# Kernel tuning notes

Hardware: AMD Instinct MI355X
Metric: run time of the kernel (lower is better)

Reference implementation:

```python
import jax, jax.numpy as jnp
import numpy as np

B, S, DIM = 2, 2048, 4096
N_HEADS, N_KV_HEADS = 32, 8
HEAD_DIM = DIM // N_HEADS  # 128
N_REP = N_HEADS // N_KV_HEADS  # 4
NEG_INF = -1e9


def setup_inputs() -> dict:
    key = jax.random.key(0)
    ks = jax.random.split(key, 6)
    x = jax.random.normal(ks[0], (B, S, DIM), dtype=jnp.float32)
    # torch Linear weights are [out_features, in_features]
    sc = 0.02
    wq = jax.random.normal(ks[1], (N_HEADS * HEAD_DIM, DIM), dtype=jnp.float32) * sc
    wk = jax.random.normal(ks[2], (N_KV_HEADS * HEAD_DIM, DIM), dtype=jnp.float32) * sc
    wv = jax.random.normal(ks[3], (N_KV_HEADS * HEAD_DIM, DIM), dtype=jnp.float32) * sc
    wo = jax.random.normal(ks[4], (DIM, N_HEADS * HEAD_DIM), dtype=jnp.float32) * sc
    # RoPE frequencies, matching llama precompute_freqs_cis (theta=10000)
    inv = 1.0 / (10000.0 ** (np.arange(0, HEAD_DIM, 2, dtype=np.float32) / HEAD_DIM))
    t = np.arange(S, dtype=np.float32)
    freqs = np.outer(t, inv)  # [S, HEAD_DIM//2]
    freqs_cos = jnp.asarray(np.cos(freqs), dtype=jnp.float32)
    freqs_sin = jnp.asarray(np.sin(freqs), dtype=jnp.float32)
    # causal mask: 0 on/below diagonal, large negative above
    mask = jnp.triu(jnp.full((S, S), NEG_INF, dtype=jnp.float32), k=1)
    return {"x": x, "wq": wq, "wk": wk, "wv": wv, "wo": wo,
            "freqs_cos": freqs_cos, "freqs_sin": freqs_sin,
            "mask": mask, "start_pos": 0}


def _apply_rope(t, cos, sin):
    # t: [b, s, h, hd]; complex mult on interleaved (even, odd) pairs
    tr, ti = t[..., 0::2], t[..., 1::2]
    cos = cos[None, :, None, :]
    sin = sin[None, :, None, :]
    out_r = tr * cos - ti * sin
    out_i = tr * sin + ti * cos
    return jnp.stack([out_r, out_i], axis=-1).reshape(t.shape)


def reference(x, wq, wk, wv, wo, freqs_cos, freqs_sin, mask, start_pos):
    bsz, seqlen, _ = x.shape
    xq = (x @ wq.T).reshape(bsz, seqlen, N_HEADS, HEAD_DIM)
    xk = (x @ wk.T).reshape(bsz, seqlen, N_KV_HEADS, HEAD_DIM)
    xv = (x @ wv.T).reshape(bsz, seqlen, N_KV_HEADS, HEAD_DIM)
    xq = _apply_rope(xq, freqs_cos, freqs_sin)
    xk = _apply_rope(xk, freqs_cos, freqs_sin)
    # prefill: start_pos == 0, so cache slice == current keys/values
    # GQA repeat_kv via broadcast (torch repeat_interleave over head dim)
    keys = jnp.broadcast_to(xk[:, :, :, None, :],
                            (bsz, seqlen, N_KV_HEADS, N_REP, HEAD_DIM)
                            ).reshape(bsz, seqlen, N_HEADS, HEAD_DIM)
    values = jnp.broadcast_to(xv[:, :, :, None, :],
                              (bsz, seqlen, N_KV_HEADS, N_REP, HEAD_DIM)
                              ).reshape(bsz, seqlen, N_HEADS, HEAD_DIM)
    scale = 1.0 / jnp.sqrt(jnp.float32(HEAD_DIM))
    # [b, h, q, k]
    scores = jnp.einsum('bqhd,bkhd->bhqk', xq, keys) * scale
    scores = scores + mask[None, None, :, :]
    probs = jax.nn.softmax(scores.astype(jnp.float32), axis=-1).astype(xq.dtype)
    out = jnp.einsum('bhqk,bkhd->bqhd', probs, values)
    out = out.reshape(bsz, seqlen, N_HEADS * HEAD_DIM)
    return out @ wo.T
```

## Files before the change

kernel.cpp:

```cpp
#include <hip/hip_runtime.h>

typedef unsigned short u16;
typedef unsigned int u32;
typedef __bf16 bf16_t;
typedef bf16_t bf16x8 __attribute__((ext_vector_type(8)));
typedef float f32x4 __attribute__((ext_vector_type(4)));

#define B_ 2
#define S_ 2048
#define DIM_ 4096
#define NH_ 32
#define NKV_ 8
#define HD_ 128

__device__ __forceinline__ u16 f2b(float f) {
  union { float f; unsigned u; } x; x.f = f;
  unsigned r = x.u + 0x7fffu + ((x.u >> 16) & 1u);
  return (u16)(r >> 16);
}
__device__ __forceinline__ float b2f(u16 u) {
  union { unsigned u; float f; } x; x.u = ((unsigned)u) << 16;
  return x.f;
}
__device__ __forceinline__ u32 cvtpk(float lo, float hi) {
  u32 r;
  asm volatile("v_cvt_pk_bf16_f32 %0, %1, %2" : "=v"(r) : "v"(lo), "v"(hi));
  return r;
}
__device__ __forceinline__ float redmax4(float x) {
  x = fmaxf(x, __shfl_xor(x, 16));
  x = fmaxf(x, __shfl_xor(x, 32));
  return x;
}
__device__ __forceinline__ float redsum4(float x) {
  x += __shfl_xor(x, 16);
  x += __shfl_xor(x, 32);
  return x;
}

#define GLDS(gsrc, ldst) \
  __builtin_amdgcn_global_load_lds((const __attribute__((address_space(1))) void*)(gsrc), \
                                   (__attribute__((address_space(3))) void*)(ldst), 16, 0, 0)
#define BAR()    __builtin_amdgcn_s_barrier()
#define SCHED0() __builtin_amdgcn_sched_barrier(0)

__global__ void cvt_kernel(const float* __restrict__ in, u16* __restrict__ out, int n4) {
  int i = blockIdx.x * blockDim.x + threadIdx.x;
  int stride = gridDim.x * blockDim.x;
  for (; i < n4; i += stride) {
    float4 v = ((const float4*)in)[i];
    ushort4 o;
    o.x = f2b(v.x); o.y = f2b(v.y); o.z = f2b(v.z); o.w = f2b(v.w);
    ((ushort4*)out)[i] = o;
  }
}

__global__ void rope_kernel(u16* __restrict__ t, const float* __restrict__ fc,
                            const float* __restrict__ fs, int nheads) {
  int idx = blockIdx.x * blockDim.x + threadIdx.x;
  int ppr = nheads * 64;
  int row = idx / ppr;
  int pr = idx - row * ppr;
  int h = pr >> 6, j = pr & 63;
  int s = row & (S_ - 1);
  float c = fc[s * 64 + j], sn = fs[s * 64 + j];
  u16* p = t + (size_t)row * (size_t)(nheads * HD_) + h * HD_ + j * 2;
  float tr = b2f(p[0]), ti = b2f(p[1]);
  p[0] = f2b(tr * c - ti * sn);
  p[1] = f2b(tr * sn + ti * c);
}

__global__ __launch_bounds__(512) void attn_kernel(const u16* __restrict__ Q,
                                                   const u16* __restrict__ Kt,
                                                   const u16* __restrict__ VT,
                                                   u16* __restrict__ O,
                                                   const float* __restrict__ fc,
                                                   const float* __restrict__ fs) {
  __shared__ u16 Ks[2][32 * 128];
  __shared__ u16 Vs[2][32 * 128];

  const int bid = blockIdx.x;
  const int qb = 15 - (bid >> 6);
  const int h = bid & 31;
  const int b = (bid >> 5) & 1;
  const int g = h >> 2;
  const int tid = threadIdx.x;
  const int lane = tid & 63;
  const int wv = tid >> 6;
  const int qrow0 = qb * 128 + wv * 16;
  const float scl2 = 0.12751744f;

  const int qloc = lane & 15;
  const int grp = lane >> 4;

  bf16x8 qf[4];
  {
    const int qr = qrow0 + qloc;
    const u16* qptr = Q + (size_t)(b * S_ + qr) * (NH_ * HD_) + h * HD_ + grp * 8;
#pragma unroll
    for (int c = 0; c < 4; c++) {
      union { bf16x8 v; u16 u[8]; } raw;
      raw.v = *(const bf16x8*)(qptr + c * 32);
      const int p0 = c * 16 + grp * 4;
      const float4 cv = *(const float4*)&fc[(size_t)qr * 64 + p0];
      const float4 sv = *(const float4*)&fs[(size_t)qr * 64 + p0];
      union { bf16x8 v; u32 w[4]; } out;
      const float cc[4] = {cv.x, cv.y, cv.z, cv.w};
      const float ss[4] = {sv.x, sv.y, sv.z, sv.w};
#pragma unroll
      for (int j = 0; j < 4; j++) {
        float tr = b2f(raw.u[2 * j]), ti = b2f(raw.u[2 * j + 1]);
        out.w[j] = cvtpk(tr * cc[j] - ti * ss[j], tr * ss[j] + ti * cc[j]);
      }
      qf[c] = out.v;
    }
  }

  float m = -1e30f, l = 0.f;
  f32x4 o[8];
#pragma unroll
  for (int c = 0; c < 8; c++)
#pragma unroll
    for (int r = 0; r < 4; r++) o[c][r] = 0.f;

  const int nkv = 4 * qb + 4;

  int ka[2][4];
#pragma unroll
  for (int n = 0; n < 2; n++)
#pragma unroll
    for (int c = 0; c < 4; c++) {
      int krow = n * 16 + qloc;
      ka[n][c] = krow * 256 + ((c * 64 + grp * 16) ^ ((krow & 7) << 4));
    }
  int va[8];
#pragma unroll
  for (int c = 0; c < 8; c++) {
    int d = c * 16 + qloc;
    va[c] = d * 64 + ((grp * 16) ^ (((d >> 1) & 3) << 4));
  }

  const int kkey = wv * 4 + grp;
  const int cbsK = (qloc * 16) ^ ((kkey & 7) << 4);
  const int vd = wv * 16 + (lane >> 2);
  const int kbsV = ((lane & 3) * 16) ^ (((vd >> 1) & 3) << 4);

  const u16* kp = Kt + (size_t)(b * S_ + kkey) * 1024 + g * HD_ + (cbsK >> 1);
  const u16* vp = VT + (size_t)(g * HD_ + vd) * 4096 + (size_t)b * S_ + (kbsV >> 1);

  GLDS(kp, &Ks[0][wv * 512]);
  GLDS(vp, &Vs[0][wv * 512]);
  kp += 32 * 1024;
  vp += 32;

#define ATTN_ITER(T, CB, NB)                                                   \
  {                                                                            \
    const bool pf = ((T) + 1 < nkv);                                           \
    if (pf) {                                                                  \
      GLDS(kp, &Ks[NB][wv * 512]);                                             \
      GLDS(vp, &Vs[NB][wv * 512]);                                             \
      asm volatile("s_waitcnt vmcnt(2)" ::: "memory");                         \
    } else {                                                                   \
      asm volatile("s_waitcnt vmcnt(0)" ::: "memory");                         \
    }                                                                          \
    BAR();                                                                     \
    SCHED0();                                                                  \
    if ((T) * 32 <= qrow0 + 15) {                                              \
      f32x4 s[2];                                                              \
      __builtin_amdgcn_s_setprio(1);                                           \
      _Pragma("unroll")                                                        \
      for (int n = 0; n < 2; n++) {                                            \
        f32x4 sc;                                                              \
        _Pragma("unroll")                                                      \
        for (int r = 0; r < 4; r++) sc[r] = 0.f;                               \
        _Pragma("unroll")                                                      \
        for (int c = 0; c < 4; c++) {                                          \
          bf16x8 kf = *(const bf16x8*)((const char*)Ks[CB] + ka[n][c]);        \
          sc = __builtin_amdgcn_mfma_f32_16x16x32_bf16(kf, qf[c], sc, 0, 0, 0);\
        }                                                                      \
        s[n] = sc;                                                             \
      }                                                                        \
      __builtin_amdgcn_s_setprio(0);                                           \
      const int q = qrow0 + qloc;                                              \
      if ((T) * 32 + 31 > qrow0) {                                             \
        _Pragma("unroll")                                                      \
        for (int n = 0; n < 2; n++)                                            \
          _Pragma("unroll")                                                    \
          for (int r = 0; r < 4; r++) {                                        \
            int k = (T) * 32 + n * 16 + grp * 4 + r;                           \
            if (k > q) s[n][r] = -1e9f;                                        \
          }                                                                    \
      }                                                                        \
      float pmax = fmaxf(fmaxf(fmaxf(s[0][0], s[0][1]), fmaxf(s[0][2], s[0][3])), \
                         fmaxf(fmaxf(s[1][0], s[1][1]), fmaxf(s[1][2], s[1][3]))); \
      pmax = redmax4(pmax);                                                    \
      if (__any(pmax > m + 64.f)) {                                            \
        float mn = fmaxf(m, pmax);                                             \
        float alpha = exp2f((m - mn) * scl2);                                  \
        m = mn;                                                                \
        l *= alpha;                                                            \
        float ar[4];                                                           \
        _Pragma("unroll")                                                      \
        for (int r = 0; r < 4; r++) ar[r] = __shfl(alpha, grp * 4 + r);        \
        _Pragma("unroll")                                                      \
        for (int c = 0; c < 8; c++)                                            \
          _Pragma("unroll")                                                    \
          for (int r = 0; r < 4; r++) o[c][r] *= ar[r];                        \
      }                                                                        \
      const float msc = m * scl2;                                              \
      float p[2][4];                                                           \
      _Pragma("unroll")                                                        \
      for (int n = 0; n < 2; n++)                                              \
        _Pragma("unroll")                                                      \
        for (int r = 0; r < 4; r++)                                            \
          p[n][r] = exp2f(fmaf(s[n][r], scl2, -msc));                          \
      float rs = ((p[0][0] + p[0][1]) + (p[0][2] + p[0][3])) +                 \
                 ((p[1][0] + p[1][1]) + (p[1][2] + p[1][3]));                  \
      l += redsum4(rs);                                                        \
      u32 a0 = cvtpk(p[0][0], p[0][1]);                                        \
      u32 a1 = cvtpk(p[0][2], p[0][3]);                                        \
      u32 b0 = cvtpk(p[1][0], p[1][1]);                                        \
      u32 b1 = cvtpk(p[1][2], p[1][3]);                                        \
      asm volatile("v_permlane32_swap_b32 %0, %1" : "+v"(a0), "+v"(b0));       \
      asm volatile("v_permlane32_swap_b32 %0, %1" : "+v"(a1), "+v"(b1));       \
      asm volatile("v_permlane16_swap_b32 %0, %1" : "+v"(a0), "+v"(b0));       \
      asm volatile("v_permlane16_swap_b32 %0, %1" : "+v"(a1), "+v"(b1));       \
      union { bf16x8 v; u32 w[4]; } pau;                                       \
      pau.w[0] = a0; pau.w[1] = a1; pau.w[2] = b0; pau.w[3] = b1;              \
      bf16x8 pa = pau.v;                                                       \
      __builtin_amdgcn_s_setprio(1);                                           \
      _Pragma("unroll")                                                        \
      for (int c = 0; c < 8; c++) {                                            \
        bf16x8 vf = *(const bf16x8*)((const char*)Vs[CB] + va[c]);             \
        o[c] = __builtin_amdgcn_mfma_f32_16x16x32_bf16(pa, vf, o[c], 0, 0, 0); \
      }                                                                        \
      __builtin_amdgcn_s_setprio(0);                                           \
    }                                                                          \
    asm volatile("s_waitcnt lgkmcnt(0)" ::: "memory");                         \
    SCHED0();                                                                  \
    BAR();                                                                     \
    kp += 32 * 1024;                                                           \
    vp += 32;                                                                  \
  }

  for (int t = 0; t < nkv; t += 2) {
    ATTN_ITER(t, 0, 1);
    ATTN_ITER(t + 1, 1, 0);
  }
#undef ATTN_ITER

  float lr[4];
#pragma unroll
  for (int r = 0; r < 4; r++) lr[r] = 1.0f / __shfl(l, grp * 4 + r);
#pragma unroll
  for (int c = 0; c < 8; c++)
#pragma unroll
    for (int r = 0; r < 4; r++) {
      int qo = qrow0 + grp * 4 + r;
      float val = o[c][r] * lr[r];
      O[(size_t)(b * S_ + qo) * (NH_ * HD_) + h * HD_ + c * 16 + qloc] = f2b(val);
    }
}

template<int MODE, bool SM>
__global__ __launch_bounds__(512, 2) void gemm256(const u16* __restrict__ A,
                                                  const u16* __restrict__ B,
                                                  void* __restrict__ Cout,
                                                  void* __restrict__ Cout2,
                                                  int M, int N, int K) {
  constexpr int BM = SM ? 128 : 256;
  constexpr int AH = SM ? 4096 : 8192;
  constexpr int II = SM ? 1 : 2;
  constexpr int NACC = SM ? 4 : 8;
  __shared__ u16 As[2][2][AH];
  __shared__ u16 Bs[2][2][8192];
  const int nbn = N >> 8;
  const int nwg = gridDim.x;
  int wg = blockIdx.x;
  wg = (wg & 7) * (nwg >> 3) + (wg >> 3);
  const int bm = wg / nbn;
  const int bn = wg - bm * nbn;
  const int tid = threadIdx.x;
  const int lane = tid & 63;
  const int wv = tid >> 6;
  const int wm = wv >> 2, wn = wv & 3;
  const int qloc = lane & 15, grp = lane >> 4;
  const int NT = K >> 6;

  f32x4 acc[NACC][4];
#pragma unroll
  for (int i = 0; i < NACC; i++)
#pragma unroll
    for (int j = 0; j < 4; j++)
#pragma unroll
      for (int r = 0; r < 4; r++) acc[i][j][r] = 0.0f;

  const int srowl = lane >> 3;
  const int scsw = 8 * ((lane & 7) ^ srowl);
  const size_t rowA = SM ? ((size_t)(bm * 128 + wv * 8 + srowl) * K + scsw)
                         : ((size_t)(bm * 256 + wv * 16 + srowl) * K + scsw);
  const size_t rowB = (size_t)(bn * 256 + wv * 16 + srowl) * K + scsw;

#define STAGE_A(buf, h, tt) { \
    if (SM) { \
      GLDS(A + rowA + (size_t)((h) * 64) * K + (size_t)(tt) * 64, &As[buf][h][wv * 512]); \
    } else { \
      GLDS(A + rowA + (size_t)((h) * 128) * K + (size_t)(tt) * 64, &As[buf][h][wv * 1024]); \
      GLDS(A + rowA + (size_t)((h) * 128 + 8) * K + (size_t)(tt) * 64, &As[buf][h][wv * 1024 + 512]); } }
#define STAGE_B(buf, h, tt) { \
    GLDS(B + rowB + (size_t)((h) * 128) * K + (size_t)(tt) * 64, &Bs[buf][h][wv * 1024]); \
    GLDS(B + rowB + (size_t)((h) * 128 + 8) * K + (size_t)(tt) * 64, &Bs[buf][h][wv * 1024 + 512]); }

  STAGE_A(0, 0, 0); STAGE_A(0, 1, 0);
  STAGE_B(0, 0, 0); STAGE_B(0, 1, 0);
  STAGE_B(1, 0, 1); STAGE_B(1, 1, 1);
  asm volatile("s_waitcnt vmcnt(4)" ::: "memory");
  BAR();

  for (int t = 0; t < NT; t += 2) {
#pragma unroll
    for (int half = 0; half < 2; half++) {
      bf16x8 bfr[4][2];
#pragma unroll
      for (int qd = 0; qd < 4; qd++) {
        if (qd == 0) {
#pragma unroll
          for (int j = 0; j < 4; j++)
#pragma unroll
            for (int ks = 0; ks < 2; ks++) {
              int rb = (wn & 1) * 64 + j * 16 + qloc;
              bfr[j][ks] = *(const bf16x8*)((const char*)&Bs[half][wn >> 1][0]
                           + rb * 128 + ((ks * 64 + grp * 16) ^ ((rb & 7) << 4)));
            }
        }
        bf16x8 af[II][2];
#pragma unroll
        for (int ii = 0; ii < II; ii++)
#pragma unroll
          for (int ks = 0; ks < 2; ks++) {
            int rh = SM ? (qd * 16 + qloc) : (qd * 32 + ii * 16 + qloc);
            af[ii][ks] = *(const bf16x8*)((const char*)&As[half][wm][0]
                         + rh * 128 + ((ks * 64 + grp * 16) ^ ((rh & 7) << 4)));
          }
        BAR();
        asm volatile("s_waitcnt lgkmcnt(0)" ::: "memory");
        SCHED0();
        __builtin_amdgcn_s_setprio(1);
#pragma unroll
        for (int ii = 0; ii < II; ii++)
#pragma unroll
          for (int ks = 0; ks < 2; ks++)
#pragma unroll
            for (int j = 0; j < 4; j++)
              acc[qd * II + ii][j] = __builtin_amdgcn_mfma_f32_16x16x32_bf16(
                  af[ii][ks], bfr[j][ks], acc[qd * II + ii][j], 0, 0, 0);
        __builtin_amdgcn_s_setprio(0);
        SCHED0();
        const int ph = half * 4 + qd;
        if (ph == 0)      { STAGE_A(1, 0, t + 1); STAGE_A(1, 1, t + 1); }
        else if (ph == 1) { if (t + 2 < NT) { STAGE_B(0, 0, t + 2); STAGE_B(0, 1, t + 2); } }
        else if (ph == 4) { if (t + 2 < NT) { STAGE_A(0, 0, t + 2); STAGE_A(0, 1, t + 2); } }
        else if (ph == 5) { if (t + 3 < NT) { STAGE_B(1, 0, t + 3); STAGE_B(1, 1, t + 3); } }
        if (qd == 3) {
          if ((half == 0 ? t + 2 : t + 3) < NT)
            asm volatile("s_waitcnt vmcnt(4)" ::: "memory");
          else
            asm volatile("s_waitcnt vmcnt(0)" ::: "memory");
          BAR();
        }
      }
    }
  }
#undef STAGE_A
#undef STAGE_B

  const int r0g = bm * BM + wm * (BM / 2) + grp * 4;
  const int c0g = bn * 256 + wn * 64 + qloc;
#pragma unroll
  for (int i = 0; i < NACC; i++)
#pragma unroll
    for (int j = 0; j < 4; j++)
#pragma unroll
      for (int r = 0; r < 4; r++) {
        int row = r0g + i * 16 + r;
        int col = c0g + j * 16;
        float v = acc[i][j][r];
        if (MODE == 1)      ((float*)Cout)[(size_t)row * N + col] = v;
        else if (MODE == 0) ((u16*)Cout)[(size_t)row * N + col]  = f2b(v);
        else {
          if (col < 1024) ((u16*)Cout)[(size_t)row * 1024 + col] = f2b(v);
          else            ((u16*)Cout2)[(size_t)(col - 1024) * M + row] = f2b(v);
        }
      }
}

extern "C" void kernel_launch(void* const* d_in, const int* in_sizes, int n_in,
                              void* d_out, int out_size, void* d_ws, size_t ws_size,
                              hipStream_t stream) {
  const float* x  = (const float*)d_in[0];
  const float* wq = (const float*)d_in[1];
  const float* wk = (const float*)d_in[2];
  const float* wv = (const float*)d_in[3];
  const float* wo = (const float*)d_in[4];
  const float* fc = (const float*)d_in[5];
  const float* fs = (const float*)d_in[6];

  char* ws = (char*)d_ws;
  u16* Xb  = (u16*)(ws);
  u16* Wqb = (u16*)(ws + 33554432);
  u16* Wkv = (u16*)(ws + 67108864);
  u16* Qw  = (u16*)(ws + 83886080);
  u16* Kw  = (u16*)(ws + 117440512);
  u16* Vw  = (u16*)(ws + 125829120);
  u16* Ow  = Xb;
  u16* Wob = Wqb;

  auto cvt = [&](const float* in, u16* out, int n) {
    int n4 = n >> 2;
    int blocks = (n4 + 255) / 256; if (blocks > 2048) blocks = 2048;
    cvt_kernel<<<dim3(blocks), dim3(256), 0, stream>>>(in, out, n4);
  };
  cvt(x,  Xb,  B_ * S_ * DIM_);
  cvt(wq, Wqb, DIM_ * DIM_);
  cvt(wk, Wkv, NKV_ * HD_ * DIM_);
  cvt(wv, Wkv + (size_t)1024 * 4096, NKV_ * HD_ * DIM_);

  gemm256<0, false><<<dim3(16 * 16), 512, 0, stream>>>(Xb, Wqb, Qw, nullptr, 4096, 4096, 4096);
  gemm256<3, true><<<dim3(32 * 8), 512, 0, stream>>>(Xb, Wkv, Kw, Vw, 4096, 2048, 4096);

  cvt(wo, Wob, DIM_ * DIM_);

  rope_kernel<<<dim3((B_ * S_ * NKV_ * 64) / 256), 256, 0, stream>>>(Kw, fc, fs, NKV_);

  attn_kernel<<<dim3(B_ * NH_ * (S_ / 128)), 512, 0, stream>>>(Qw, Kw, Vw, Ow, fc, fs);

  gemm256<1, false><<<dim3(16 * 16), 512, 0, stream>>>(Ow, Wob, d_out, nullptr, 4096, 4096, 4096);
}
```

Before: 505.5 us.

## Double KV tile size in attention kernel from 32 to 64 keys

The flash-attention loop now processes 64 keys per iteration instead of 32, so it stages twice as much K and V into shared memory per step and runs half as many iterations. Each barrier pair, softmax rescale check and reduction now covers twice the work, which cuts per-iteration synchronisation and overhead. In exchange it uses more LDS and registers (4 score tiles, 2 P fragments), which may lower occupancy. It also wastes more masked work on the causal diagonal.

```diff
diff --git a/kernel.cpp b/kernel.cpp
--- a/kernel.cpp
+++ b/kernel.cpp
@@ -76,8 +76,8 @@
                                                    u16* __restrict__ O,
                                                    const float* __restrict__ fc,
                                                    const float* __restrict__ fs) {
-  __shared__ u16 Ks[2][32 * 128];
-  __shared__ u16 Vs[2][32 * 128];
+  __shared__ u16 Ks[2][64 * 128];
+  __shared__ u16 Vs[2][128 * 64];
 
   const int bid = blockIdx.x;
   const int qb = 15 - (bid >> 6);
@@ -123,76 +123,81 @@
 #pragma unroll
     for (int r = 0; r < 4; r++) o[c][r] = 0.f;
 
-  const int nkv = 4 * qb + 4;
-
-  int ka[2][4];
-#pragma unroll
-  for (int n = 0; n < 2; n++)
-#pragma unroll
-    for (int c = 0; c < 4; c++) {
-      int krow = n * 16 + qloc;
-      ka[n][c] = krow * 256 + ((c * 64 + grp * 16) ^ ((krow & 7) << 4));
+  const int nkv = 2 * qb + 2;
+
+  int ka[4];
+#pragma unroll
+  for (int c = 0; c < 4; c++)
+    ka[c] = qloc * 256 + ((c * 64 + grp * 16) ^ ((qloc & 7) << 4));
+  int va[2][8];
+#pragma unroll
+  for (int s = 0; s < 2; s++)
+#pragma unroll
+    for (int c = 0; c < 8; c++) {
+      int d = c * 16 + qloc;
+      va[s][c] = d * 128 + (((s * 64) | (grp * 16)) ^ ((d & 7) << 4));
     }
-  int va[8];
-#pragma unroll
-  for (int c = 0; c < 8; c++) {
-    int d = c * 16 + qloc;
-    va[c] = d * 64 + ((grp * 16) ^ (((d >> 1) & 3) << 4));
-  }
 
   const int kkey = wv * 4 + grp;
   const int cbsK = (qloc * 16) ^ ((kkey & 7) << 4);
-  const int vd = wv * 16 + (lane >> 2);
-  const int kbsV = ((lane & 3) * 16) ^ (((vd >> 1) & 3) << 4);
+  const int vd = wv * 8 + (lane >> 3);
+  const int cbsV = ((lane & 7) * 16) ^ (((lane >> 3) & 7) << 4);
 
   const u16* kp = Kt + (size_t)(b * S_ + kkey) * 1024 + g * HD_ + (cbsK >> 1);
-  const u16* vp = VT + (size_t)(g * HD_ + vd) * 4096 + (size_t)b * S_ + (kbsV >> 1);
-
-  GLDS(kp, &Ks[0][wv * 512]);
-  GLDS(vp, &Vs[0][wv * 512]);
-  kp += 32 * 1024;
-  vp += 32;
+  const u16* vp = VT + (size_t)(g * HD_ + vd) * 4096 + (size_t)b * S_ + (cbsV >> 1);
+
+#define STAGE_KV(T, buf) { \
+    GLDS(kp,              &Ks[buf][wv * 512]); \
+    GLDS(kp + 32 * 1024,  &Ks[buf][(8 + wv) * 512]); \
+    GLDS(vp,              &Vs[buf][wv * 512]); \
+    GLDS(vp + 64 * 4096,  &Vs[buf][(8 + wv) * 512]); \
+    kp += 64 * 1024; \
+    vp += 64; }
+
+  STAGE_KV(0, 0)
 
 #define ATTN_ITER(T, CB, NB)                                                   \
   {                                                                            \
     const bool pf = ((T) + 1 < nkv);                                           \
     if (pf) {                                                                  \
-      GLDS(kp, &Ks[NB][wv * 512]);                                             \
-      GLDS(vp, &Vs[NB][wv * 512]);                                             \
-      asm volatile("s_waitcnt vmcnt(2)" ::: "memory");                         \
+      STAGE_KV((T) + 1, NB)                                                    \
+      asm volatile("s_waitcnt vmcnt(4)" ::: "memory");                         \
     } else {                                                                   \
       asm volatile("s_waitcnt vmcnt(0)" ::: "memory");                         \
     }                                                                          \
     BAR();                                                                     \
     SCHED0();                                                                  \
-    if ((T) * 32 <= qrow0 + 15) {                                              \
-      f32x4 s[2];                                                              \
+    if ((T) * 64 <= qrow0 + 15) {                                              \
+      f32x4 s[4];                                                              \
       __builtin_amdgcn_s_setprio(1);                                           \
       _Pragma("unroll")                                                        \
-      for (int n = 0; n < 2; n++) {                                            \
+      for (int n = 0; n < 4; n++) {                                            \
         f32x4 sc;                                                              \
         _Pragma("unroll")                                                      \
         for (int r = 0; r < 4; r++) sc[r] = 0.f;                               \
         _Pragma("unroll")                                                      \
         for (int c = 0; c < 4; c++) {                                          \
-          bf16x8 kf = *(const bf16x8*)((const char*)Ks[CB] + ka[n][c]);        \
+          bf16x8 kf = *(const bf16x8*)((const char*)Ks[CB] + ka[c] + n * 4096);\
           sc = __builtin_amdgcn_mfma_f32_16x16x32_bf16(kf, qf[c], sc, 0, 0, 0);\
         }                                                                      \
         s[n] = sc;                                                             \
       }                                                                        \
       __builtin_amdgcn_s_setprio(0);                                           \
       const int q = qrow0 + qloc;                                              \
-      if ((T) * 32 + 31 > qrow0) {                                             \
-        _Pragma("unroll")                                                      \
-        for (int n = 0; n < 2; n++)                                            \
+      if ((T) * 64 + 63 > qrow0) {                                             \
+        _Pragma("unroll")                                                      \
+        for (int n = 0; n < 4; n++)                                            \
           _Pragma("unroll")                                                    \
           for (int r = 0; r < 4; r++) {                                        \
-            int k = (T) * 32 + n * 16 + grp * 4 + r;                           \
+            int k = (T) * 64 + n * 16 + grp * 4 + r;                           \
             if (k > q) s[n][r] = -1e9f;                                        \
           }                                                                    \
       }                                                                        \
       float pmax = fmaxf(fmaxf(fmaxf(s[0][0], s[0][1]), fmaxf(s[0][2], s[0][3])), \
                          fmaxf(fmaxf(s[1][0], s[1][1]), fmaxf(s[1][2], s[1][3]))); \
+      pmax = fmaxf(pmax,                                                       \
+             fmaxf(fmaxf(fmaxf(s[2][0], s[2][1]), fmaxf(s[2][2], s[2][3])),    \
+                   fmaxf(fmaxf(s[3][0], s[3][1]), fmaxf(s[3][2], s[3][3]))));  \
       pmax = redmax4(pmax);                                                    \
       if (__any(pmax > m + 64.f)) {                                            \
         float mn = fmaxf(m, pmax);                                             \
@@ -208,39 +213,45 @@
           for (int r = 0; r < 4; r++) o[c][r] *= ar[r];                        \
       }                                                                        \
       const float msc = m * scl2;                                              \
-      float p[2][4];                                                           \
+      float p[4][4];                                                           \
       _Pragma("unroll")                                                        \
-      for (int n = 0; n < 2; n++)                                              \
+      for (int n = 0; n < 4; n++)                                              \
         _Pragma("unroll")                                                      \
         for (int r = 0; r < 4; r++)                                            \
           p[n][r] = exp2f(fmaf(s[n][r], scl2, -msc));                          \
-      float rs = ((p[0][0] + p[0][1]) + (p[0][2] + p[0][3])) +                 \
-                 ((p[1][0] + p[1][1]) + (p[1][2] + p[1][3]));                  \
+      float rs = (((p[0][0] + p[0][1]) + (p[0][2] + p[0][3])) +                \
+                  ((p[1][0] + p[1][1]) + (p[1][2] + p[1][3]))) +               \
+                 (((p[2][0] + p[2][1]) + (p[2][2] + p[2][3])) +                \
+                  ((p[3][0] + p[3][1]) + (p[3][2] + p[3][3])));                \
       l += redsum4(rs);                                                        \
-      u32 a0 = cvtpk(p[0][0], p[0][1]);                                        \
-      u32 a1 = cvtpk(p[0][2], p[0][3]);                                        \
-      u32 b0 = cvtpk(p[1][0], p[1][1]);                                        \
-      u32 b1 = cvtpk(p[1][2], p[1][3]);                                        \
-      asm volatile("v_permlane32_swap_b32 %0, %1" : "+v"(a0), "+v"(b0));       \
-      asm volatile("v_permlane32_swap_b32 %0, %1" : "+v"(a1), "+v"(b1));       \
-      asm volatile("v_permlane16_swap_b32 %0, %1" : "+v"(a0), "+v"(b0));       \
-      asm volatile("v_permlane16_swap_b32 %0, %1" : "+v"(a1), "+v"(b1));       \
-      union { bf16x8 v; u32 w[4]; } pau;                                       \
-      pau.w[0] = a0; pau.w[1] = a1; pau.w[2] = b0; pau.w[3] = b1;              \
-      bf16x8 pa = pau.v;                                                       \
+      bf16x8 pa[2];                                                            \
+      _Pragma("unroll")                                                        \
+      for (int sl = 0; sl < 2; sl++) {                                         \
+        u32 a0 = cvtpk(p[2 * sl][0], p[2 * sl][1]);                            \
+        u32 a1 = cvtpk(p[2 * sl][2], p[2 * sl][3]);                            \
+        u32 b0 = cvtpk(p[2 * sl + 1][0], p[2 * sl + 1][1]);                    \
+        u32 b1 = cvtpk(p[2 * sl + 1][2], p[2 * sl + 1][3]);                    \
+        asm volatile("v_permlane32_swap_b32 %0, %1" : "+v"(a0), "+v"(b0));     \
+        asm volatile("v_permlane32_swap_b32 %0, %1" : "+v"(a1), "+v"(b1));     \
+        asm volatile("v_permlane16_swap_b32 %0, %1" : "+v"(a0), "+v"(b0));     \
+        asm volatile("v_permlane16_swap_b32 %0, %1" : "+v"(a1), "+v"(b1));     \
+        union { bf16x8 v; u32 w[4]; } pau;                                     \
+        pau.w[0] = a0; pau.w[1] = a1; pau.w[2] = b0; pau.w[3] = b1;            \
+        pa[sl] = pau.v;                                                        \
+      }                                                                        \
       __builtin_amdgcn_s_setprio(1);                                           \
       _Pragma("unroll")                                                        \
       for (int c = 0; c < 8; c++) {                                            \
-        bf16x8 vf = *(const bf16x8*)((const char*)Vs[CB] + va[c]);             \
-        o[c] = __builtin_amdgcn_mfma_f32_16x16x32_bf16(pa, vf, o[c], 0, 0, 0); \
+        bf16x8 vf0 = *(const bf16x8*)((const char*)Vs[CB] + va[0][c]);         \
+        bf16x8 vf1 = *(const bf16x8*)((const char*)Vs[CB] + va[1][c]);         \
+        o[c] = __builtin_amdgcn_mfma_f32_16x16x32_bf16(pa[0], vf0, o[c], 0, 0, 0); \
+        o[c] = __builtin_amdgcn_mfma_f32_16x16x32_bf16(pa[1], vf1, o[c], 0, 0, 0); \
       }                                                                        \
       __builtin_amdgcn_s_setprio(0);                                           \
     }                                                                          \
     asm volatile("s_waitcnt lgkmcnt(0)" ::: "memory");                         \
     SCHED0();                                                                  \
     BAR();                                                                     \
-    kp += 32 * 1024;                                                           \
-    vp += 32;                                                                  \
   }
 
   for (int t = 0; t < nkv; t += 2) {
@@ -248,6 +259,7 @@
     ATTN_ITER(t + 1, 1, 0);
   }
 #undef ATTN_ITER
+#undef STAGE_KV
 
   float lr[4];
 #pragma unroll
```

Result: no change. 504.6 us (-0.2%).
